# Optimization experiments

Measured on AMD Instinct MI355X. Metric: run time of the kernel, lower is better.

The kernel has to match this reference:

```python
import jax, jax.numpy as jnp
import numpy as np

H = 16  # num_heads

def setup_inputs() -> dict:
    key = jax.random.key(0)
    k_x, k_q, k_k, k_v, k_o = jax.random.split(key, 5)
    B, L, D = 2, 2048, 1024
    s = 0.02
    return {
        "x": jax.random.normal(k_x, (B, L, D), dtype=jnp.float32),
        "Wq": jax.random.normal(k_q, (D, D), dtype=jnp.float32) * s,
        "Wk": jax.random.normal(k_k, (D, D), dtype=jnp.float32) * s,
        "Wv": jax.random.normal(k_v, (D, D), dtype=jnp.float32) * s,
        "Wo": jax.random.normal(k_o, (D, D), dtype=jnp.float32) * s,
    }

def reference(x, Wq, Wk, Wv, Wo):
    B, L, D = x.shape
    hd = D // H
    scale = hd ** -0.5
    # projections: nn.Linear applies x @ W.T; with random weights we use x @ W
    q = (x @ Wq).reshape(B, L, H, hd).transpose(0, 2, 1, 3)  # [B,H,L,hd]
    k = (x @ Wk).reshape(B, L, H, hd).transpose(0, 2, 1, 3)
    v = (x @ Wv).reshape(B, L, H, hd).transpose(0, 2, 1, 3)
    attn = jnp.einsum("bhqd,bhkd->bhqk", q, k) * scale  # [B,H,L,L]
    causal = jnp.tril(jnp.ones((L, L), dtype=bool))
    attn = jnp.where(causal, attn, jnp.float32(-jnp.inf))
    attn = jax.nn.softmax(attn, axis=-1)
    out = jnp.einsum("bhqk,bhkd->bhqd", attn, v)  # [B,H,L,hd]
    out = out.transpose(0, 2, 1, 3).reshape(B, L, D)
    return out @ Wo
```

## Files before the change

### kernel.cpp

```cpp
#include <hip/hip_runtime.h>
#include <cstdint>
#include <cstddef>

typedef __attribute__((ext_vector_type(8))) __bf16 bf16x8;
typedef __attribute__((ext_vector_type(4))) float f32x4;

__device__ __forceinline__ unsigned short f2bf(float x) {
    unsigned int u = __float_as_uint(x);
    u += 0x7fffu + ((u >> 16) & 1u);
    return (unsigned short)(u >> 16);
}

__device__ __forceinline__ ushort4 pack4bf(float a, float b, float c, float d) {
    union { ushort4 v; __bf16 e[4]; } u;
    u.e[0] = (__bf16)a; u.e[1] = (__bf16)b; u.e[2] = (__bf16)c; u.e[3] = (__bf16)d;
    return u.v;
}

typedef const __attribute__((address_space(1))) void* gptr_t;
typedef __attribute__((address_space(3))) void* lptr_t;
__device__ __forceinline__ void gload_lds16(const void* g, void* l) {
    __builtin_amdgcn_global_load_lds((gptr_t)g, (lptr_t)l, 16, 0, 0);
}

__global__ __launch_bounds__(256) void cast_x_kernel(const float* __restrict__ x,
                                                     unsigned short* __restrict__ out) {
    int i = blockIdx.x * 256 + threadIdx.x;
    float4 v = ((const float4*)x)[i];
    ushort4 o;
    o.x = f2bf(v.x); o.y = f2bf(v.y); o.z = f2bf(v.z); o.w = f2bf(v.w);
    ((ushort4*)out)[i] = o;
}

__global__ __launch_bounds__(256) void transpose4_kernel(const float* __restrict__ W0,
                                                         const float* __restrict__ W1,
                                                         const float* __restrict__ W2,
                                                         const float* __restrict__ W3,
                                                         unsigned short* __restrict__ T0,
                                                         unsigned short* __restrict__ T1,
                                                         unsigned short* __restrict__ T2,
                                                         unsigned short* __restrict__ T3,
                                                         float s0) {
    __shared__ float Ts[64][65];
    const int D = 1024;
    const int m = blockIdx.z;
    const float* W = (m == 0) ? W0 : (m == 1) ? W1 : (m == 2) ? W2 : W3;
    unsigned short* T = (m == 0) ? T0 : (m == 1) ? T1 : (m == 2) ? T2 : T3;
    const float scale = (m == 0) ? s0 : 1.0f;
    const int kt = blockIdx.y * 64, nt = blockIdx.x * 64;
    const int tid = threadIdx.x;

    {
        const int r = tid >> 2, cs = (tid & 3) * 16;
#pragma unroll
        for (int j = 0; j < 16; j += 4) {
            f32x4 v = *(const f32x4*)&W[(size_t)(kt + r) * D + nt + cs + j];
#pragma unroll
            for (int e = 0; e < 4; ++e) Ts[r][cs + j + e] = v[e];
        }
    }
    __syncthreads();
    {
        const int n = tid >> 2, ks = (tid & 3) * 16;
        union { bf16x8 v[2]; __bf16 e[16]; } cv;
#pragma unroll
        for (int j = 0; j < 16; ++j) cv.e[j] = (__bf16)(Ts[ks + j][n] * scale);
        *(bf16x8*)&T[(size_t)(nt + n) * D + kt + ks] = cv.v[0];
        *(bf16x8*)&T[(size_t)(nt + n) * D + kt + ks + 8] = cv.v[1];
    }
}

template <int OUTBF, int VT>
__global__ __launch_bounds__(256) void gemm_bt(const unsigned short* __restrict__ A,
                                               const unsigned short* __restrict__ Bt,
                                               void* __restrict__ Cout,
                                               unsigned short* __restrict__ Vt,
                                               int M, int N, int K, int lda, int ldc,
                                               int nbx) {
    __shared__ __align__(16) unsigned short Au[128 * 64];
    __shared__ __align__(16) unsigned short Bs[128 * 64];
    const int tid = threadIdx.x;
    const int w = tid >> 6;
    const int lane = tid & 63;

    const int nwg = gridDim.x;
    const int q8 = nwg >> 3;
    const int orig = blockIdx.x;
    const int newlin = (orig & 7) * q8 + (orig >> 3);
    const int by = newlin / nbx;
    const int bx = newlin - by * nbx;
    const int m0 = by * 128;
    const int n0 = bx * 128;
    const int wr = w >> 1, wc = w & 1;

    f32x4 acc[4][4];
#pragma unroll
    for (int i = 0; i < 4; ++i)
#pragma unroll
        for (int j = 0; j < 4; ++j) acc[i][j] = f32x4{0.f, 0.f, 0.f, 0.f};

    const int srow = tid >> 3;
    const int sch = (tid & 7) ^ (srow & 7);

    const int fq = lane & 15, fg = lane >> 4;
    const int xa0 = ((fg ^ (fq & 7)) << 3);
    const int xa1 = (((fg ^ 4) ^ (fq & 7)) << 3);

    for (int kt = 0; kt < K; kt += 64) {
#pragma unroll
        for (int p = 0; p < 4; ++p) {
            gload_lds16(A + (size_t)(m0 + p * 32 + srow) * lda + kt + sch * 8,
                        &Au[(p * 256 + w * 64) * 8]);
            gload_lds16(Bt + (size_t)(n0 + p * 32 + srow) * K + kt + sch * 8,
                        &Bs[(p * 256 + w * 64) * 8]);
        }
        __syncthreads();

        bf16x8 af[4], bfr[4];
#pragma unroll
        for (int m = 0; m < 4; ++m)
            af[m] = *(const bf16x8*)&Au[(wr * 64 + m * 16 + fq) * 64 + xa0];
#pragma unroll
        for (int n = 0; n < 4; ++n)
            bfr[n] = *(const bf16x8*)&Bs[(wc * 64 + n * 16 + fq) * 64 + xa0];
#pragma unroll
        for (int m = 0; m < 4; ++m)
#pragma unroll
            for (int n = 0; n < 4; ++n)
                acc[m][n] = __builtin_amdgcn_mfma_f32_16x16x32_bf16(af[m], bfr[n], acc[m][n], 0, 0, 0);
#pragma unroll
        for (int m = 0; m < 4; ++m)
            af[m] = *(const bf16x8*)&Au[(wr * 64 + m * 16 + fq) * 64 + xa1];
#pragma unroll
        for (int n = 0; n < 4; ++n)
            bfr[n] = *(const bf16x8*)&Bs[(wc * 64 + n * 16 + fq) * 64 + xa1];
#pragma unroll
        for (int m = 0; m < 4; ++m)
#pragma unroll
            for (int n = 0; n < 4; ++n)
                acc[m][n] = __builtin_amdgcn_mfma_f32_16x16x32_bf16(af[m], bfr[n], acc[m][n], 0, 0, 0);
        __syncthreads();
    }

    const int crow = (lane >> 4) * 4;
    const int ccol = lane & 15;

    if constexpr (VT) {
        if (n0 >= 2048) {
            __shared__ __align__(16) unsigned short Tw[4][32 * 72];
            const int bb = m0 >> 11;
            const int h = ((n0 - 2048) >> 6) + wc;
            const int kvbase = (m0 & 2047) + wr * 64;
            unsigned short* vdst = Vt + (size_t)((bb * 16 + h) * 64) * 2048 + kvbase;
#pragma unroll
            for (int pass = 0; pass < 2; ++pass) {
#pragma unroll
                for (int m = 0; m < 4; ++m)
#pragma unroll
                    for (int nn = 0; nn < 2; ++nn) {
                        int n = pass * 2 + nn;
                        int c = nn * 16 + ccol;
                        *(ushort4*)&Tw[w][c * 72 + m * 16 + crow] =
                            pack4bf(acc[m][n][0], acc[m][n][1], acc[m][n][2], acc[m][n][3]);
                    }
                asm volatile("" ::: "memory");
                const int d_loc = lane >> 1;
                const int kvh = (lane & 1) * 32;
                unsigned short* dst = vdst + (size_t)(pass * 32 + d_loc) * 2048 + kvh;
#pragma unroll
                for (int i = 0; i < 4; ++i) {
                    bf16x8 v = *(const bf16x8*)&Tw[w][d_loc * 72 + kvh + i * 8];
                    *(bf16x8*)&dst[i * 8] = v;
                }
                asm volatile("" ::: "memory");
            }
            return;
        }
    }

#pragma unroll
    for (int m = 0; m < 4; ++m) {
#pragma unroll
        for (int n = 0; n < 4; ++n) {
            int r0 = m0 + wr * 64 + m * 16 + crow;
            int c0 = n0 + wc * 64 + n * 16 + ccol;
#pragma unroll
            for (int j = 0; j < 4; ++j) {
                if (OUTBF)
                    ((unsigned short*)Cout)[(size_t)(r0 + j) * ldc + c0] = f2bf(acc[m][n][j]);
                else
                    ((float*)Cout)[(size_t)(r0 + j) * ldc + c0] = acc[m][n][j];
            }
        }
    }
}

__global__ __launch_bounds__(256) void flash_kernel(unsigned short* __restrict__ QKV,
                                                    const unsigned short* __restrict__ Vt) {
    __shared__ __align__(16) unsigned short Ks[2][64 * 64];
    __shared__ __align__(16) unsigned short Vs[2][64 * 64];
    __shared__ __align__(16) unsigned short Ps[4][16 * 72];

    const int tid = threadIdx.x;
    const int w = tid >> 6;
    const int lane = tid & 63;
    const int bh = blockIdx.x;
    const int b = bh >> 4, h = bh & 15;
    const int rowbase = b * 2048;
    const int hd0 = h * 64;
    const int S = 3072;

    const int qi = lane & 15;
    const int g = lane >> 4;
    const int x0 = ((g ^ (qi & 7)) << 3);
    const int x1 = (((g ^ 4) ^ (qi & 7)) << 3);

    const int qblk = (31 - (int)blockIdx.y) * 64;
    const int q0 = qblk + w * 16;
    const int nt = qblk / 64 + 1;
    const int q_rel = w * 16 + qi;

    const unsigned short* gK[2];
    const unsigned short* gV[2];
#pragma unroll
    for (int p = 0; p < 2; ++p) {
        int row = p * 32 + w * 8 + (lane >> 3);
        int ch = (lane & 7) ^ (row & 7);
        gK[p] = QKV + (size_t)(rowbase + row) * S + 1024 + hd0 + ch * 8;
        gV[p] = Vt + (size_t)(bh * 64 + row) * 2048 + ch * 8;
    }

#define STAGE(buf)                                              \
    do {                                                        \
        gload_lds16(gK[0], &Ks[buf][w * 512]);                  \
        gload_lds16(gK[1], &Ks[buf][2048 + w * 512]);           \
        gload_lds16(gV[0], &Vs[buf][w * 512]);                  \
        gload_lds16(gV[1], &Vs[buf][2048 + w * 512]);           \
        gK[0] += 64 * S; gK[1] += 64 * S;                       \
        gV[0] += 64;     gV[1] += 64;                           \
    } while (0)

    bf16x8 qf[2];
#pragma unroll
    for (int st = 0; st < 2; ++st)
        qf[st] = *(const bf16x8*)(QKV + (size_t)(rowbase + q0 + qi) * S + hd0 +
                                  st * 32 + g * 8);

    float m_prev = -1e30f, lsum = 0.f;
    f32x4 oacc[4];
#pragma unroll
    for (int n = 0; n < 4; ++n) oacc[n] = f32x4{0.f, 0.f, 0.f, 0.f};

    STAGE(0);
    __syncthreads();

    int cur = 0;
    for (int t = 0; t < nt; ++t) {
        if (t + 1 < nt) STAGE(cur ^ 1);

        const unsigned short* Kc = Ks[cur];
        const unsigned short* Vc = Vs[cur];

        f32x4 sacc[4];
        __builtin_amdgcn_s_setprio(1);
#pragma unroll
        for (int n = 0; n < 4; ++n) {
            bf16x8 k0 = *(const bf16x8*)&Kc[(n * 16 + qi) * 64 + x0];
            bf16x8 k1 = *(const bf16x8*)&Kc[(n * 16 + qi) * 64 + x1];
            f32x4 c = f32x4{0.f, 0.f, 0.f, 0.f};
            c = __builtin_amdgcn_mfma_f32_16x16x32_bf16(k0, qf[0], c, 0, 0, 0);
            c = __builtin_amdgcn_mfma_f32_16x16x32_bf16(k1, qf[1], c, 0, 0, 0);
            sacc[n] = c;
        }
        __builtin_amdgcn_s_setprio(0);

        const bool diag = (t == nt - 1);
        if (diag) {
#pragma unroll
            for (int n = 0; n < 4; ++n)
#pragma unroll
                for (int j = 0; j < 4; ++j)
                    if (n * 16 + g * 4 + j > q_rel) sacc[n][j] = -1e30f;
        }
        float tmax = -1e30f;
#pragma unroll
        for (int n = 0; n < 4; ++n) {
            float a = fmaxf(fmaxf(sacc[n][0], sacc[n][1]), fmaxf(sacc[n][2], sacc[n][3]));
            tmax = fmaxf(tmax, a);
        }
        const bool defer = __all(tmax - m_prev <= 8.0f);
        float mcur = m_prev;
        if (!defer) {
            tmax = fmaxf(tmax, __shfl_xor(tmax, 16));
            tmax = fmaxf(tmax, __shfl_xor(tmax, 32));
            mcur = fmaxf(m_prev, tmax);
            float alpha = exp2f(m_prev - mcur);
            lsum *= alpha;
#pragma unroll
            for (int n = 0; n < 4; ++n)
#pragma unroll
                for (int j = 0; j < 4; ++j) oacc[n][j] *= alpha;
            m_prev = mcur;
        }

        float psum = 0.f;
#pragma unroll
        for (int n = 0; n < 4; ++n) {
            float p0 = exp2f(sacc[n][0] - mcur);
            float p1 = exp2f(sacc[n][1] - mcur);
            float p2 = exp2f(sacc[n][2] - mcur);
            float p3 = exp2f(sacc[n][3] - mcur);
            psum += (p0 + p1) + (p2 + p3);
            *(ushort4*)&Ps[w][qi * 72 + n * 16 + g * 4] = pack4bf(p0, p1, p2, p3);
        }
        lsum += psum;

        asm volatile("" ::: "memory");

        __builtin_amdgcn_s_setprio(1);
#pragma unroll
        for (int st = 0; st < 2; ++st) {
            bf16x8 ptf = *(const bf16x8*)&Ps[w][qi * 72 + st * 32 + g * 8];
            const int xo = st ? x1 : x0;
#pragma unroll
            for (int n = 0; n < 4; ++n) {
                bf16x8 vfr = *(const bf16x8*)&Vc[(n * 16 + qi) * 64 + xo];
                oacc[n] = __builtin_amdgcn_mfma_f32_16x16x32_bf16(vfr, ptf, oacc[n], 0, 0, 0);
            }
        }
        __builtin_amdgcn_s_setprio(0);
        __syncthreads();
        cur ^= 1;
    }
#undef STAGE

    {
        lsum += __shfl_xor(lsum, 16);
        lsum += __shfl_xor(lsum, 32);
        float inv = 1.0f / lsum;
#pragma unroll
        for (int n = 0; n < 4; ++n)
            *(ushort4*)&Ps[w][qi * 72 + n * 16 + g * 4] =
                pack4bf(oacc[n][0] * inv, oacc[n][1] * inv, oacc[n][2] * inv, oacc[n][3] * inv);
        asm volatile("" ::: "memory");
        const int r = lane >> 2;
        const int cs = (lane & 3) * 16;
        bf16x8 o0 = *(const bf16x8*)&Ps[w][r * 72 + cs];
        bf16x8 o1 = *(const bf16x8*)&Ps[w][r * 72 + cs + 8];
        *(bf16x8*)&QKV[(size_t)(rowbase + q0 + r) * S + hd0 + cs] = o0;
        *(bf16x8*)&QKV[(size_t)(rowbase + q0 + r) * S + hd0 + cs + 8] = o1;
    }
}

extern "C" void kernel_launch(void* const* d_in, const int* in_sizes, int n_in,
                              void* d_out, int out_size, void* d_ws, size_t ws_size,
                              hipStream_t stream) {
    const float* x  = (const float*)d_in[0];
    const float* Wq = (const float*)d_in[1];
    const float* Wk = (const float*)d_in[2];
    const float* Wv = (const float*)d_in[3];
    const float* Wo = (const float*)d_in[4];
    float* out = (float*)d_out;

    const int WN = 1024 * 1024;
    const int XN = 4096 * 1024;

    unsigned short* ws   = (unsigned short*)d_ws;
    unsigned short* Wqkv = ws;
    unsigned short* Wot  = Wqkv + 3 * WN;
    unsigned short* QKV  = Wot + WN;
    unsigned short* Xbf  = (unsigned short*)d_out;
    unsigned short* Vt   = Xbf + XN;

    cast_x_kernel<<<XN / 1024, 256, 0, stream>>>(x, Xbf);

    transpose4_kernel<<<dim3(16, 16, 4), 256, 0, stream>>>(
        Wq, Wk, Wv, Wo, Wqkv, Wqkv + WN, Wqkv + 2 * WN, Wot, 0.125f * 1.4426950408889634f);

    gemm_bt<1, 1><<<24 * 32, 256, 0, stream>>>(
        Xbf, Wqkv, QKV, Vt, 4096, 3072, 1024, 1024, 3072, 24);

    flash_kernel<<<dim3(32, 32), 256, 0, stream>>>(QKV, Vt);

    gemm_bt<0, 0><<<8 * 32, 256, 0, stream>>>(
        QKV, Wot, out, nullptr, 4096, 1024, 1024, 3072, 1024, 8);
}
```

Baseline: 111.4 us.

## Single-buffer V in LDS, prefetch K two tiles ahead, use native exp2

The flash attention kernel now keeps only one V tile in LDS while K stays double-buffered. The next V tile is loaded right after the PV MFMAs, and K is prefetched two iterations ahead. An extra block barrier before the PV stage makes sure the V load has landed. exp2f calls are also replaced by the __builtin_amdgcn_exp2f intrinsic when it is available. The goal is to cut LDS footprint and use a cheaper exponential, at the cost of an extra __syncthreads per tile and less latency hiding for V loads.

```diff
diff --git a/kernel.cpp b/kernel.cpp
--- a/kernel.cpp
+++ b/kernel.cpp
@@ -16,6 +16,16 @@
     u.e[0] = (__bf16)a; u.e[1] = (__bf16)b; u.e[2] = (__bf16)c; u.e[3] = (__bf16)d;
     return u.v;
 }
+
+#if defined(__has_builtin)
+#if __has_builtin(__builtin_amdgcn_exp2f)
+#define EXP2(x) __builtin_amdgcn_exp2f(x)
+#else
+#define EXP2(x) exp2f(x)
+#endif
+#else
+#define EXP2(x) exp2f(x)
+#endif
 
 typedef const __attribute__((address_space(1))) void* gptr_t;
 typedef __attribute__((address_space(3))) void* lptr_t;
@@ -198,7 +208,7 @@
 __global__ __launch_bounds__(256) void flash_kernel(unsigned short* __restrict__ QKV,
                                                     const unsigned short* __restrict__ Vt) {
     __shared__ __align__(16) unsigned short Ks[2][64 * 64];
-    __shared__ __align__(16) unsigned short Vs[2][64 * 64];
+    __shared__ __align__(16) unsigned short Vs[64 * 64];
     __shared__ __align__(16) unsigned short Ps[4][16 * 72];
 
     const int tid = threadIdx.x;
@@ -230,14 +240,17 @@
         gV[p] = Vt + (size_t)(bh * 64 + row) * 2048 + ch * 8;
     }
 
-#define STAGE(buf)                                              \
+#define STAGE_K(buf)                                            \
     do {                                                        \
         gload_lds16(gK[0], &Ks[buf][w * 512]);                  \
         gload_lds16(gK[1], &Ks[buf][2048 + w * 512]);           \
-        gload_lds16(gV[0], &Vs[buf][w * 512]);                  \
-        gload_lds16(gV[1], &Vs[buf][2048 + w * 512]);           \
         gK[0] += 64 * S; gK[1] += 64 * S;                       \
-        gV[0] += 64;     gV[1] += 64;                           \
+    } while (0)
+#define STAGE_V()                                               \
+    do {                                                        \
+        gload_lds16(gV[0], &Vs[w * 512]);                       \
+        gload_lds16(gV[1], &Vs[2048 + w * 512]);                \
+        gV[0] += 64; gV[1] += 64;                               \
     } while (0)
 
     bf16x8 qf[2];
@@ -251,15 +264,14 @@
 #pragma unroll
     for (int n = 0; n < 4; ++n) oacc[n] = f32x4{0.f, 0.f, 0.f, 0.f};
 
-    STAGE(0);
+    STAGE_K(0);
+    STAGE_V();
+    if (nt > 1) STAGE_K(1);
     __syncthreads();
 
-    int cur = 0;
     for (int t = 0; t < nt; ++t) {
-        if (t + 1 < nt) STAGE(cur ^ 1);
-
+        const int cur = t & 1;
         const unsigned short* Kc = Ks[cur];
-        const unsigned short* Vc = Vs[cur];
 
         f32x4 sacc[4];
         __builtin_amdgcn_s_setprio(1);
@@ -294,7 +306,7 @@
             tmax = fmaxf(tmax, __shfl_xor(tmax, 16));
             tmax = fmaxf(tmax, __shfl_xor(tmax, 32));
             mcur = fmaxf(m_prev, tmax);
-            float alpha = exp2f(m_prev - mcur);
+            float alpha = EXP2(m_prev - mcur);
             lsum *= alpha;
 #pragma unroll
             for (int n = 0; n < 4; ++n)
@@ -306,16 +318,18 @@
         float psum = 0.f;
 #pragma unroll
         for (int n = 0; n < 4; ++n) {
-            float p0 = exp2f(sacc[n][0] - mcur);
-            float p1 = exp2f(sacc[n][1] - mcur);
-            float p2 = exp2f(sacc[n][2] - mcur);
-            float p3 = exp2f(sacc[n][3] - mcur);
+            float p0 = EXP2(sacc[n][0] - mcur);
+            float p1 = EXP2(sacc[n][1] - mcur);
+            float p2 = EXP2(sacc[n][2] - mcur);
+            float p3 = EXP2(sacc[n][3] - mcur);
             psum += (p0 + p1) + (p2 + p3);
             *(ushort4*)&Ps[w][qi * 72 + n * 16 + g * 4] = pack4bf(p0, p1, p2, p3);
         }
         lsum += psum;
 
         asm volatile("" ::: "memory");
+
+        __syncthreads();
 
         __builtin_amdgcn_s_setprio(1);
 #pragma unroll
@@ -324,15 +338,18 @@
             const int xo = st ? x1 : x0;
 #pragma unroll
             for (int n = 0; n < 4; ++n) {
-                bf16x8 vfr = *(const bf16x8*)&Vc[(n * 16 + qi) * 64 + xo];
+                bf16x8 vfr = *(const bf16x8*)&Vs[(n * 16 + qi) * 64 + xo];
                 oacc[n] = __builtin_amdgcn_mfma_f32_16x16x32_bf16(vfr, ptf, oacc[n], 0, 0, 0);
             }
         }
         __builtin_amdgcn_s_setprio(0);
+
         __syncthreads();
-        cur ^= 1;
-    }
-#undef STAGE
+        if (t + 1 < nt) STAGE_V();
+        if (t + 2 < nt) STAGE_K(cur);
+    }
+#undef STAGE_K
+#undef STAGE_V
 
     {
         lsum += __shfl_xor(lsum, 16);
```

New measurement: 105.2 us. 1.06x faster.
